# Performance work log

Measured on AMD Instinct MI355X. Metric: run time of the kernel, lower is better.

Reference implementation:

```python
import jax, jax.numpy as jnp
import numpy as np

B, CIN, H, W = 2, 3, 768, 768
CB = 32          # backbone out_channels (= channels_mid for heads)
ORDER = 5
MARGIN = 3.0     # ScaledTanh margin of refinement head


def _conv(x, w, b, pad):
    # x: [N,C,H,W], w: [O,I,kh,kw]
    y = jax.lax.conv_general_dilated(x, w, (1, 1), [(pad, pad), (pad, pad)],
                                     dimension_numbers=('NCHW', 'OIHW', 'NCHW'))
    return y + b[None, :, None, None]


def _readout(x, w1, b1, s, t, w2, b2, pad):
    # conv(k) -> batchnorm(eval, folded to scale/shift) -> relu -> dropout(eval=id) -> conv1x1
    h = _conv(x, w1, b1, pad)
    h = jax.nn.relu(h * s[None, :, None, None] + t[None, :, None, None])
    return _conv(h, w2, b2, 0)


def setup_inputs() -> dict:
    key = jax.random.key(0)
    ks = iter(jax.random.split(key, 16))
    def rn(shape, scale=0.05):
        return jax.random.normal(next(ks), shape, jnp.float32) * scale
    d = {'inputs': jax.random.normal(next(ks), (B, CIN, H, W), jnp.float32)}
    d['bb_w'] = rn((CB, CIN, 3, 3)); d['bb_b'] = jnp.zeros((CB,), jnp.float32)
    def head(name, k, cout):
        d[name + '_w1'] = rn((CB, CB, k, k)); d[name + '_b1'] = jnp.zeros((CB,), jnp.float32)
        d[name + '_s'] = jnp.ones((CB,), jnp.float32); d[name + '_t'] = jnp.zeros((CB,), jnp.float32)
        d[name + '_w2'] = rn((cout, CB, 1, 1)); d[name + '_b2'] = jnp.zeros((cout,), jnp.float32)
    head('score', 3, 2)
    head('loc', 7, 2)
    head('four', 7, ORDER * 4)
    head('ref', 7, 2)
    return d


def reference(inputs, bb_w, bb_b,
              score_w1, score_b1, score_s, score_t, score_w2, score_b2,
              loc_w1, loc_b1, loc_s, loc_t, loc_w2, loc_b2,
              four_w1, four_b1, four_s, four_t, four_w2, four_b2,
              ref_w1, ref_b1, ref_s, ref_t, ref_w2, ref_b2):
    # backbone (simple conv + relu; out_channels is an int so contour == refinement features)
    feats = jax.nn.relu(_conv(inputs, bb_w, bb_b, 1))
    scores = _readout(feats, score_w1, score_b1, score_s, score_t, score_w2, score_b2, 1)
    locations = _readout(feats, loc_w1, loc_b1, loc_s, loc_t, loc_w2, loc_b2, 3)
    fourier = _readout(feats, four_w1, four_b1, four_s, four_t, four_w2, four_b2, 3)
    # ReadOut final activation ScaledTanh(3.0), then CPNCore multiplies by internal margin 1.0;
    # feature HW == input HW (stride 1), so F.interpolate is a no-op.
    refinement = jnp.tanh(_readout(feats, ref_w1, ref_b1, ref_s, ref_t, ref_w2, ref_b2, 3)) * MARGIN
    return (scores, locations, refinement, fourier)
```

## Files before the change

### kernel.cpp

```cpp
#include <hip/hip_runtime.h>
#include <hip/hip_bf16.h>
#include <cmath>

#define HH 768
#define WW 768
#define HWSZ (768*768)

typedef __attribute__((ext_vector_type(8))) short bhalf8;
typedef __attribute__((ext_vector_type(4))) float f32x4;

__device__ inline ushort f2bf(float f) {
  __hip_bfloat16 h = __float2bfloat16(f);
  return *reinterpret_cast<ushort*>(&h);
}

__global__ __launch_bounds__(256) void wxform_kernel(
    const float* __restrict__ w1, const float* __restrict__ b1,
    const float* __restrict__ s,  const float* __restrict__ t,
    ushort* __restrict__ wT, float* __restrict__ bb, int npos)
{
  int i = blockIdx.x * 256 + threadIdx.x;
  if (i < npos * 1024) {
    int pos = i >> 10, mc = i & 1023, m = mc >> 5, c = mc & 31;
    wT[i] = f2bf(w1[(m * 32 + c) * npos + pos] * s[m]);
  }
  if (i < 32) bb[i] = b1[i] * s[i] + t[i];
}

__global__ __launch_bounds__(256) void backbone_kernel(
    const float* __restrict__ x, const float* __restrict__ w,
    const float* __restrict__ bias, ushort* __restrict__ feats)
{
  int p = blockIdx.x * 256 + threadIdx.x;
  int bb  = p / HWSZ;
  int rem = p - bb * HWSZ;
  int y   = rem / WW;
  int xx  = rem - y * WW;
  const float* xb = x + (size_t)bb * 3 * HWSZ;

  float v[3][3][3];
  #pragma unroll
  for (int c = 0; c < 3; c++)
    #pragma unroll
    for (int dy = 0; dy < 3; dy++)
      #pragma unroll
      for (int dx = 0; dx < 3; dx++) {
        int yy = y + dy - 1, xq = xx + dx - 1;
        v[c][dy][dx] = (yy >= 0 && yy < HH && xq >= 0 && xq < WW)
                         ? xb[(size_t)c * HWSZ + yy * WW + xq] : 0.f;
      }

  union { ushort u[32]; uint4 q[4]; } pk;
  #pragma unroll
  for (int o = 0; o < 32; o++) {
    float acc = bias[o];
    #pragma unroll
    for (int c = 0; c < 3; c++)
      #pragma unroll
      for (int dy = 0; dy < 3; dy++)
        #pragma unroll
        for (int dx = 0; dx < 3; dx++)
          acc = fmaf(w[((o * 3 + c) * 3 + dy) * 3 + dx], v[c][dy][dx], acc);
    pk.u[o] = f2bf(fmaxf(acc, 0.f));
  }
  uint4* dst = (uint4*)(feats + ((size_t)bb * HWSZ + rem) * 32);
  #pragma unroll
  for (int i = 0; i < 4; i++) dst[i] = pk.q[i];
}

template <int K, int COUT, bool DO_TANH>
__global__ __launch_bounds__(256) void head_mfma_kernel(
    const ushort* __restrict__ feats,
    const ushort* __restrict__ wT,
    const float*  __restrict__ bbias,
    const float*  __restrict__ w2, const float* __restrict__ b2,
    float* __restrict__ out)
{
  constexpr int PAD  = K / 2;
  constexpr int TW   = 16 + 2 * PAD;
  constexpr int NPIX = TW * TW;
  constexpr int CPAD = 40;
  constexpr int SMEM_BYTES = (NPIX * CPAD * 2 > 256 * 33 * 4) ? NPIX * CPAD * 2
                                                              : 256 * 33 * 4;
  __shared__ __align__(16) char smem[SMEM_BYTES];
  ushort* tile = (ushort*)smem;

  int bx = blockIdx.x % 48;
  int by = (blockIdx.x / 48) % 48;
  int bb = blockIdx.x / (48 * 48);
  int x0 = bx * 16 - PAD, y0 = by * 16 - PAD;

  const ushort* fB = feats + (size_t)bb * HWSZ * 32;

  for (int p = threadIdx.x; p < NPIX; p += 256) {
    int py = p / TW, px = p % TW;
    int yy = y0 + py, xx = x0 + px;
    uint4 q0 = {0,0,0,0}, q1 = {0,0,0,0}, q2 = {0,0,0,0}, q3 = {0,0,0,0};
    if (yy >= 0 && yy < HH && xx >= 0 && xx < WW) {
      const uint4* src = (const uint4*)(fB + ((size_t)yy * WW + xx) * 32);
      q0 = src[0]; q1 = src[1]; q2 = src[2]; q3 = src[3];
    }
    uint4* dst = (uint4*)(tile + (size_t)p * CPAD);
    dst[0] = q0; dst[1] = q1; dst[2] = q2; dst[3] = q3;
  }
  __syncthreads();

  int l  = threadIdx.x & 63;
  int wv = threadIdx.x >> 6;
  int px = l & 15;
  int g  = l >> 4;

  f32x4 acc[2][4] = {};

  for (int ky = 0; ky < K; ky++) {
    bhalf8 areg[K][2];
    #pragma unroll
    for (int kx = 0; kx < K; kx++)
      #pragma unroll
      for (int mh = 0; mh < 2; mh++)
        areg[kx][mh] = *(const bhalf8*)(wT + (size_t)(ky * K + kx) * 1024
                                           + mh * 512 + px * 32 + g * 8);
    #pragma unroll
    for (int kx = 0; kx < K; kx++) {
      #pragma unroll
      for (int i = 0; i < 4; i++) {
        int pgrow = wv * 4 + i;
        const bhalf8 bfrag = *(const bhalf8*)(
            tile + (size_t)((pgrow + ky) * TW + px + kx) * CPAD + g * 8);
        acc[0][i] = __builtin_amdgcn_mfma_f32_16x16x32_bf16(areg[kx][0], bfrag, acc[0][i], 0, 0, 0);
        acc[1][i] = __builtin_amdgcn_mfma_f32_16x16x32_bf16(areg[kx][1], bfrag, acc[1][i], 0, 0, 0);
      }
    }
  }

  __syncthreads();
  float* mid = (float*)smem;
  #pragma unroll
  for (int mh = 0; mh < 2; mh++)
    #pragma unroll
    for (int i = 0; i < 4; i++) {
      int pgrow = wv * 4 + i;
      #pragma unroll
      for (int r = 0; r < 4; r++) {
        int m = mh * 16 + g * 4 + r;
        int pix = pgrow * 16 + px;
        mid[pix * 33 + m] = fmaxf(acc[mh][i][r] + bbias[m], 0.f);
      }
    }
  __syncthreads();

  int pix = threadIdx.x;
  int py  = pix >> 4, pxl = pix & 15;
  int oy  = by * 16 + py, ox = bx * 16 + pxl;
  size_t opix = (size_t)oy * WW + ox;
  float* ob = out + (size_t)bb * COUT * HWSZ;

  float m_[32];
  #pragma unroll
  for (int m = 0; m < 32; m++) m_[m] = mid[pix * 33 + m];

  #pragma unroll
  for (int oc = 0; oc < COUT; oc++) {
    float acc2 = b2[oc];
    #pragma unroll
    for (int m = 0; m < 32; m++) acc2 = fmaf(w2[oc * 32 + m], m_[m], acc2);
    if (DO_TANH) acc2 = tanhf(acc2) * 3.0f;
    ob[(size_t)oc * HWSZ + opix] = acc2;
  }
}

extern "C" void kernel_launch(void* const* d_in, const int* in_sizes, int n_in,
                              void* d_out, int out_size, void* d_ws, size_t ws_size,
                              hipStream_t stream) {
  const float* input = (const float*)d_in[0];
  const float* bb_w  = (const float*)d_in[1];
  const float* bb_b  = (const float*)d_in[2];

  ushort* feats = (ushort*)d_ws;
  char* base = (char*)d_ws;
  const size_t FEATS_BYTES = (size_t)2 * HWSZ * 32 * 2;
  const size_t WT_STRIDE   = 49 * 1024 * 2;
  ushort* wT0 = (ushort*)(base + FEATS_BYTES);
  float*  bb0 = (float*)(base + FEATS_BYTES + 4 * WT_STRIDE);
  (void)out_size; (void)ws_size; (void)n_in; (void)in_sizes;

  float* out = (float*)d_out;
  const size_t SCORES_OFF = 0;
  const size_t LOC_OFF    = (size_t)2 * 2 * HWSZ;
  const size_t REF_OFF    = (size_t)2 * 2 * HWSZ * 2;
  const size_t FOUR_OFF   = (size_t)2 * 2 * HWSZ * 3;

  const int npos_h[4] = {9, 49, 49, 49};
  for (int h = 0; h < 4; h++) {
    const float* w1 = (const float*)d_in[3 + h * 6 + 0];
    const float* b1 = (const float*)d_in[3 + h * 6 + 1];
    const float* s  = (const float*)d_in[3 + h * 6 + 2];
    const float* t  = (const float*)d_in[3 + h * 6 + 3];
    ushort* wT = (ushort*)((char*)wT0 + h * WT_STRIDE);
    float*  bbv = bb0 + h * 32;
    int n = npos_h[h] * 1024;
    wxform_kernel<<<(n + 255) / 256, 256, 0, stream>>>(w1, b1, s, t, wT, bbv, npos_h[h]);
  }

  backbone_kernel<<<4608, 256, 0, stream>>>(input, bb_w, bb_b, feats);

  const int HEAD_GRID = 2 * 48 * 48;

  head_mfma_kernel<3, 2, false><<<HEAD_GRID, 256, 0, stream>>>(
      feats, (ushort*)((char*)wT0 + 0 * WT_STRIDE), bb0 + 0 * 32,
      (const float*)d_in[7], (const float*)d_in[8], out + SCORES_OFF);

  head_mfma_kernel<7, 2, false><<<HEAD_GRID, 256, 0, stream>>>(
      feats, (ushort*)((char*)wT0 + 1 * WT_STRIDE), bb0 + 1 * 32,
      (const float*)d_in[13], (const float*)d_in[14], out + LOC_OFF);

  head_mfma_kernel<7, 20, false><<<HEAD_GRID, 256, 0, stream>>>(
      feats, (ushort*)((char*)wT0 + 2 * WT_STRIDE), bb0 + 2 * 32,
      (const float*)d_in[19], (const float*)d_in[20], out + FOUR_OFF);

  head_mfma_kernel<7, 2, true><<<HEAD_GRID, 256, 0, stream>>>(
      feats, (ushort*)((char*)wT0 + 3 * WT_STRIDE), bb0 + 3 * 32,
      (const float*)d_in[25], (const float*)d_in[26], out + REF_OFF);
}
```

Measured before the change: 497.2 us.

## Fuse four readout heads into one kernel sharing a feature tile with 32x32 MFMA

Replaces four separate head launches with one kernel that loads the 22x22 bf16 feature tile once and computes all four heads' first convolutions from the same B fragments. The 3x3 score head reuses the center taps of the 7x7 loop. It also switches from 16x16x32 to 32x32x16 MFMA, so each wave covers all 32 output channels. This removes three redundant feature-tile loads and three launches. In exchange the kernel carries four sets of 32-wide accumulators (high register pressure, likely lower occupancy) and runs four serialized epilogues that reuse shared memory.

```diff
diff --git a/kernel.cpp b/kernel.cpp
--- a/kernel.cpp
+++ b/kernel.cpp
@@ -8,6 +8,7 @@
 
 typedef __attribute__((ext_vector_type(8))) short bhalf8;
 typedef __attribute__((ext_vector_type(4))) float f32x4;
+typedef __attribute__((ext_vector_type(16))) float f32x16;
 
 __device__ inline ushort f2bf(float f) {
   __hip_bfloat16 h = __float2bfloat16(f);
@@ -68,33 +69,71 @@
   for (int i = 0; i < 4; i++) dst[i] = pk.q[i];
 }
 
-template <int K, int COUT, bool DO_TANH>
-__global__ __launch_bounds__(256) void head_mfma_kernel(
+template <int COUT, bool DO_TANH>
+__device__ inline void head_epilogue(
+    const f32x16 acc[2], const float* __restrict__ bbh,
+    const float* __restrict__ w2, const float* __restrict__ b2,
+    float* __restrict__ outh, float* mid,
+    int wv, int qr, int qc, int kg, int by, int bx)
+{
+  #pragma unroll
+  for (int n = 0; n < 2; n++) {
+    int pix = (wv * 4 + 2 * n + qr) * 16 + qc;
+    #pragma unroll
+    for (int rg = 0; rg < 4; rg++) {
+      int m0 = 8 * rg + 4 * kg;
+      f32x4 v;
+      #pragma unroll
+      for (int j = 0; j < 4; j++)
+        v[j] = fmaxf(acc[n][rg * 4 + j] + bbh[m0 + j], 0.f);
+      *(f32x4*)(mid + pix * 36 + m0) = v;
+    }
+  }
+  __syncthreads();
+
+  int t = threadIdx.x;
+  float mv[32];
+  #pragma unroll
+  for (int j2 = 0; j2 < 8; j2++)
+    *(f32x4*)(mv + 4 * j2) = *(const f32x4*)(mid + t * 36 + 4 * j2);
+
+  int oy = by * 16 + (t >> 4), ox = bx * 16 + (t & 15);
+  size_t opix = (size_t)oy * WW + ox;
+  #pragma unroll
+  for (int oc = 0; oc < COUT; oc++) {
+    float a2 = b2[oc];
+    #pragma unroll
+    for (int m = 0; m < 32; m++) a2 = fmaf(w2[oc * 32 + m], mv[m], a2);
+    if (DO_TANH) a2 = tanhf(a2) * 3.0f;
+    outh[(size_t)oc * HWSZ + opix] = a2;
+  }
+  __syncthreads();
+}
+
+__global__ __launch_bounds__(256) void fused_heads_kernel(
     const ushort* __restrict__ feats,
-    const ushort* __restrict__ wT,
-    const float*  __restrict__ bbias,
-    const float*  __restrict__ w2, const float* __restrict__ b2,
+    const ushort* __restrict__ wtS, const ushort* __restrict__ wtL,
+    const ushort* __restrict__ wtF, const ushort* __restrict__ wtR,
+    const float*  __restrict__ bb0,
+    const float* __restrict__ w2S, const float* __restrict__ b2S,
+    const float* __restrict__ w2L, const float* __restrict__ b2L,
+    const float* __restrict__ w2F, const float* __restrict__ b2F,
+    const float* __restrict__ w2R, const float* __restrict__ b2R,
     float* __restrict__ out)
 {
-  constexpr int PAD  = K / 2;
-  constexpr int TW   = 16 + 2 * PAD;
-  constexpr int NPIX = TW * TW;
-  constexpr int CPAD = 40;
-  constexpr int SMEM_BYTES = (NPIX * CPAD * 2 > 256 * 33 * 4) ? NPIX * CPAD * 2
-                                                              : 256 * 33 * 4;
-  __shared__ __align__(16) char smem[SMEM_BYTES];
+  constexpr int TW = 22, CPAD = 40;
+  __shared__ __align__(16) char smem[TW * TW * CPAD * 2];
   ushort* tile = (ushort*)smem;
 
   int bx = blockIdx.x % 48;
   int by = (blockIdx.x / 48) % 48;
-  int bb = blockIdx.x / (48 * 48);
-  int x0 = bx * 16 - PAD, y0 = by * 16 - PAD;
-
+  int bb = blockIdx.x / 2304;
+  int x0 = bx * 16 - 3, y0 = by * 16 - 3;
   const ushort* fB = feats + (size_t)bb * HWSZ * 32;
 
-  for (int p = threadIdx.x; p < NPIX; p += 256) {
-    int py = p / TW, px = p % TW;
-    int yy = y0 + py, xx = x0 + px;
+  for (int p = threadIdx.x; p < TW * TW; p += 256) {
+    int py = p / TW, pxx = p % TW;
+    int yy = y0 + py, xx = x0 + pxx;
     uint4 q0 = {0,0,0,0}, q1 = {0,0,0,0}, q2 = {0,0,0,0}, q3 = {0,0,0,0};
     if (yy >= 0 && yy < HH && xx >= 0 && xx < WW) {
       const uint4* src = (const uint4*)(fB + ((size_t)yy * WW + xx) * 32);
@@ -107,66 +146,72 @@
 
   int l  = threadIdx.x & 63;
   int wv = threadIdx.x >> 6;
-  int px = l & 15;
-  int g  = l >> 4;
-
-  f32x4 acc[2][4] = {};
-
-  for (int ky = 0; ky < K; ky++) {
-    bhalf8 areg[K][2];
-    #pragma unroll
-    for (int kx = 0; kx < K; kx++)
-      #pragma unroll
-      for (int mh = 0; mh < 2; mh++)
-        areg[kx][mh] = *(const bhalf8*)(wT + (size_t)(ky * K + kx) * 1024
-                                           + mh * 512 + px * 32 + g * 8);
-    #pragma unroll
-    for (int kx = 0; kx < K; kx++) {
-      #pragma unroll
-      for (int i = 0; i < 4; i++) {
-        int pgrow = wv * 4 + i;
-        const bhalf8 bfrag = *(const bhalf8*)(
-            tile + (size_t)((pgrow + ky) * TW + px + kx) * CPAD + g * 8);
-        acc[0][i] = __builtin_amdgcn_mfma_f32_16x16x32_bf16(areg[kx][0], bfrag, acc[0][i], 0, 0, 0);
-        acc[1][i] = __builtin_amdgcn_mfma_f32_16x16x32_bf16(areg[kx][1], bfrag, acc[1][i], 0, 0, 0);
+  int q  = l & 31;
+  int kg = l >> 5;
+  int qr = q >> 4, qc = q & 15;
+
+  const ushort* pb = tile + ((wv * 4 + qr) * TW + qc) * CPAD + kg * 8;
+  const int aoff = q * 32 + kg * 8;
+
+  f32x16 accS[2] = {};
+  f32x16 accL[2] = {};
+  f32x16 accF[2] = {};
+  f32x16 accR[2] = {};
+
+  #pragma unroll
+  for (int ky = 0; ky < 7; ky++) {
+    #pragma unroll
+    for (int kx = 0; kx < 7; kx++) {
+      const int tap = ky * 7 + kx;
+      bhalf8 aL[2], aF[2], aR[2];
+      #pragma unroll
+      for (int kh = 0; kh < 2; kh++) {
+        aL[kh] = *(const bhalf8*)(wtL + tap * 1024 + aoff + kh * 16);
+        aF[kh] = *(const bhalf8*)(wtF + tap * 1024 + aoff + kh * 16);
+        aR[kh] = *(const bhalf8*)(wtR + tap * 1024 + aoff + kh * 16);
+      }
+      bhalf8 bfr[2][2];
+      #pragma unroll
+      for (int n = 0; n < 2; n++)
+        #pragma unroll
+        for (int kh = 0; kh < 2; kh++)
+          bfr[n][kh] = *(const bhalf8*)(pb + (ky * TW + kx) * CPAD + n * 2 * TW * CPAD + kh * 16);
+
+      #pragma unroll
+      for (int n = 0; n < 2; n++)
+        #pragma unroll
+        for (int kh = 0; kh < 2; kh++) {
+          accL[n] = __builtin_amdgcn_mfma_f32_32x32x16_bf16(aL[kh], bfr[n][kh], accL[n], 0, 0, 0);
+          accF[n] = __builtin_amdgcn_mfma_f32_32x32x16_bf16(aF[kh], bfr[n][kh], accF[n], 0, 0, 0);
+          accR[n] = __builtin_amdgcn_mfma_f32_32x32x16_bf16(aR[kh], bfr[n][kh], accR[n], 0, 0, 0);
+        }
+
+      if (ky >= 2 && ky <= 4 && kx >= 2 && kx <= 4) {
+        const int stap = (ky - 2) * 3 + (kx - 2);
+        bhalf8 aS[2];
+        #pragma unroll
+        for (int kh = 0; kh < 2; kh++)
+          aS[kh] = *(const bhalf8*)(wtS + stap * 1024 + aoff + kh * 16);
+        #pragma unroll
+        for (int n = 0; n < 2; n++)
+          #pragma unroll
+          for (int kh = 0; kh < 2; kh++)
+            accS[n] = __builtin_amdgcn_mfma_f32_32x32x16_bf16(aS[kh], bfr[n][kh], accS[n], 0, 0, 0);
       }
     }
   }
 
   __syncthreads();
   float* mid = (float*)smem;
-  #pragma unroll
-  for (int mh = 0; mh < 2; mh++)
-    #pragma unroll
-    for (int i = 0; i < 4; i++) {
-      int pgrow = wv * 4 + i;
-      #pragma unroll
-      for (int r = 0; r < 4; r++) {
-        int m = mh * 16 + g * 4 + r;
-        int pix = pgrow * 16 + px;
-        mid[pix * 33 + m] = fmaxf(acc[mh][i][r] + bbias[m], 0.f);
-      }
-    }
-  __syncthreads();
-
-  int pix = threadIdx.x;
-  int py  = pix >> 4, pxl = pix & 15;
-  int oy  = by * 16 + py, ox = bx * 16 + pxl;
-  size_t opix = (size_t)oy * WW + ox;
-  float* ob = out + (size_t)bb * COUT * HWSZ;
-
-  float m_[32];
-  #pragma unroll
-  for (int m = 0; m < 32; m++) m_[m] = mid[pix * 33 + m];
-
-  #pragma unroll
-  for (int oc = 0; oc < COUT; oc++) {
-    float acc2 = b2[oc];
-    #pragma unroll
-    for (int m = 0; m < 32; m++) acc2 = fmaf(w2[oc * 32 + m], m_[m], acc2);
-    if (DO_TANH) acc2 = tanhf(acc2) * 3.0f;
-    ob[(size_t)oc * HWSZ + opix] = acc2;
-  }
+
+  head_epilogue<2,  false>(accS, bb0 +  0, w2S, b2S,
+                           out + (size_t)bb * 2  * HWSZ,                     mid, wv, qr, qc, kg, by, bx);
+  head_epilogue<2,  false>(accL, bb0 + 32, w2L, b2L,
+                           out + (size_t)4  * HWSZ + (size_t)bb * 2  * HWSZ, mid, wv, qr, qc, kg, by, bx);
+  head_epilogue<20, false>(accF, bb0 + 64, w2F, b2F,
+                           out + (size_t)12 * HWSZ + (size_t)bb * 20 * HWSZ, mid, wv, qr, qc, kg, by, bx);
+  head_epilogue<2,  true >(accR, bb0 + 96, w2R, b2R,
+                           out + (size_t)8  * HWSZ + (size_t)bb * 2  * HWSZ, mid, wv, qr, qc, kg, by, bx);
 }
 
 extern "C" void kernel_launch(void* const* d_in, const int* in_sizes, int n_in,
@@ -185,10 +230,6 @@
   (void)out_size; (void)ws_size; (void)n_in; (void)in_sizes;
 
   float* out = (float*)d_out;
-  const size_t SCORES_OFF = 0;
-  const size_t LOC_OFF    = (size_t)2 * 2 * HWSZ;
-  const size_t REF_OFF    = (size_t)2 * 2 * HWSZ * 2;
-  const size_t FOUR_OFF   = (size_t)2 * 2 * HWSZ * 3;
 
   const int npos_h[4] = {9, 49, 49, 49};
   for (int h = 0; h < 4; h++) {
@@ -204,21 +245,16 @@
 
   backbone_kernel<<<4608, 256, 0, stream>>>(input, bb_w, bb_b, feats);
 
-  const int HEAD_GRID = 2 * 48 * 48;
-
-  head_mfma_kernel<3, 2, false><<<HEAD_GRID, 256, 0, stream>>>(
-      feats, (ushort*)((char*)wT0 + 0 * WT_STRIDE), bb0 + 0 * 32,
-      (const float*)d_in[7], (const float*)d_in[8], out + SCORES_OFF);
-
-  head_mfma_kernel<7, 2, false><<<HEAD_GRID, 256, 0, stream>>>(
-      feats, (ushort*)((char*)wT0 + 1 * WT_STRIDE), bb0 + 1 * 32,
-      (const float*)d_in[13], (const float*)d_in[14], out + LOC_OFF);
-
-  head_mfma_kernel<7, 20, false><<<HEAD_GRID, 256, 0, stream>>>(
-      feats, (ushort*)((char*)wT0 + 2 * WT_STRIDE), bb0 + 2 * 32,
-      (const float*)d_in[19], (const float*)d_in[20], out + FOUR_OFF);
-
-  head_mfma_kernel<7, 2, true><<<HEAD_GRID, 256, 0, stream>>>(
-      feats, (ushort*)((char*)wT0 + 3 * WT_STRIDE), bb0 + 3 * 32,
-      (const float*)d_in[25], (const float*)d_in[26], out + REF_OFF);
-}
+  fused_heads_kernel<<<2 * 48 * 48, 256, 0, stream>>>(
+      feats,
+      (const ushort*)((char*)wT0 + 0 * WT_STRIDE),
+      (const ushort*)((char*)wT0 + 1 * WT_STRIDE),
+      (const ushort*)((char*)wT0 + 2 * WT_STRIDE),
+      (const ushort*)((char*)wT0 + 3 * WT_STRIDE),
+      bb0,
+      (const float*)d_in[7],  (const float*)d_in[8],
+      (const float*)d_in[13], (const float*)d_in[14],
+      (const float*)d_in[19], (const float*)d_in[20],
+      (const float*)d_in[25], (const float*)d_in[26],
+      out);
+}
```

Result: slower. 546.5 us (+9.9%).
